# Performance work log

Measured on AMD Instinct MI355X. Metric: run time of the kernel, lower is better.

## Reference

```python
import jax, jax.numpy as jnp
import numpy as np

B = 512      # graphs per batch
NPG = 62     # nodes (electrodes) per graph
N = B * NPG  # total nodes per band
F_IN = 5     # node features
H = 8        # attention heads
C = 3        # num_classes (GATConv out channels, concat=False)
DEG = 16     # avg degree
EG = NPG * DEG
E = B * EG   # edges per band
NB = 5       # bands: delta, alpha, beta, theta, gamma
DE_DIM = 930 # 310*3


def setup_inputs() -> dict:
    key = jax.random.key(0)
    ks = jax.random.split(key, 24)
    x_bands = jax.random.normal(ks[0], (NB, N, F_IN), dtype=jnp.float32)
    # within-graph random edges: node ids in [g*62, g*62+62)
    base = (jnp.arange(B, dtype=jnp.int32) * NPG)[None, :, None]
    src = jax.random.randint(ks[1], (NB, B, EG), 0, NPG, dtype=jnp.int32) + base
    dst = jax.random.randint(ks[2], (NB, B, EG), 0, NPG, dtype=jnp.int32) + base
    edge_index_bands = jnp.stack([src.reshape(NB, E), dst.reshape(NB, E)], axis=1)  # [NB,2,E]
    batch = jnp.repeat(jnp.arange(B, dtype=jnp.int32), NPG)  # [N]
    de = jax.random.normal(ks[3], (B, NPG, 5, 3), dtype=jnp.float32)
    s = 0.3
    params = dict(
        bn_gamma=jnp.ones((NB, F_IN), jnp.float32),
        bn_beta=jnp.zeros((NB, F_IN), jnp.float32),
        W=jax.random.normal(ks[4], (NB, F_IN, H * C)) * s,
        att_src=jax.random.normal(ks[5], (NB, H, C)) * s,
        att_dst=jax.random.normal(ks[6], (NB, H, C)) * s,
        gat_bias=jax.random.normal(ks[7], (NB, C)) * 0.01,
        fg_W=jax.random.normal(ks[8], (NB * C, 64)) * s,
        fg_b=jnp.zeros((64,), jnp.float32),
        ln_g=jnp.ones((DE_DIM,), jnp.float32),
        ln_b=jnp.zeros((DE_DIM,), jnp.float32),
        q_W=jax.random.normal(ks[9], (DE_DIM, 64)) * 0.03,
        q_b=jnp.zeros((64,), jnp.float32),
        k_W=jax.random.normal(ks[10], (DE_DIM, 64)) * 0.03,
        k_b=jnp.zeros((64,), jnp.float32),
        v_W=jax.random.normal(ks[11], (DE_DIM, 64)) * 0.03,
        v_b=jnp.zeros((64,), jnp.float32),
        fa_W=jax.random.normal(ks[12], (128, C)) * s,
        fa_b=jnp.zeros((C,), jnp.float32),
    )
    return dict(x_bands=x_bands, edge_index_bands=edge_index_bands, batch=batch, de=de, **params)


def _gat_band(x, ei, g, b, Wb, a_src, a_dst, bias, batch):
    # BatchNorm1d (training-mode batch stats), eps=1e-5
    mu = x.mean(0)
    var = x.var(0)
    xn = (x - mu) * jax.lax.rsqrt(var + 1e-5) * g + b
    # GATConv(F_IN -> C, heads=H, concat=False) with self-loops
    xt = (xn @ Wb).reshape(N, H, C)                       # [N,H,C]
    al_s = (xt * a_src).sum(-1)                           # [N,H]
    al_d = (xt * a_dst).sum(-1)                           # [N,H]
    loop = jnp.arange(N, dtype=ei.dtype)
    src = jnp.concatenate([ei[0], loop])                  # [E+N]
    dst = jnp.concatenate([ei[1], loop])
    e = jax.nn.leaky_relu(al_s[src] + al_d[dst], 0.2)     # [E+N,H]
    m = jax.ops.segment_max(e, dst, num_segments=N)
    ex = jnp.exp(e - m[dst])
    denom = jax.ops.segment_sum(ex, dst, num_segments=N)  # [N,H]
    msg = ex[:, :, None] * xt[src]                        # [E+N,H,C]
    out = jax.ops.segment_sum(msg, dst, num_segments=N) / denom[:, :, None]
    out = out.mean(1) + bias                              # concat=False -> head mean
    out = jax.nn.elu(out)
    # global_mean_pool
    summed = jax.ops.segment_sum(out, batch, num_segments=B)
    cnt = jax.ops.segment_sum(jnp.ones((N,), out.dtype), batch, num_segments=B)
    return summed / cnt[:, None]                          # [B,C]


def reference(x_bands, edge_index_bands, batch, de, bn_gamma, bn_beta, W,
              att_src, att_dst, gat_bias, fg_W, fg_b, ln_g, ln_b,
              q_W, q_b, k_W, k_b, v_W, v_b, fa_W, fa_b):
    pooled = jax.vmap(_gat_band, in_axes=(0, 0, 0, 0, 0, 0, 0, 0, None))(
        x_bands, edge_index_bands, bn_gamma, bn_beta, W, att_src, att_dst, gat_bias, batch
    )  # [NB,B,C]
    x_concat = jnp.transpose(pooled, (1, 0, 2)).reshape(B, NB * C)  # [B,15]
    x_out = jax.nn.elu(x_concat @ fg_W + fg_b)                       # [B,64]
    # de branch: LayerNorm + self-attention
    de_f = de.reshape(B, DE_DIM)
    mu = de_f.mean(-1, keepdims=True)
    var = de_f.var(-1, keepdims=True)
    de_n = (de_f - mu) * jax.lax.rsqrt(var + 1e-5) * ln_g + ln_b
    Q = de_n @ q_W + q_b
    K = de_n @ k_W + k_b
    V = de_n @ v_W + v_b
    attn = jax.nn.softmax(Q @ K.T / jnp.sqrt(jnp.float32(64)), axis=-1)
    x_de = attn @ V                                                  # [B,64]
    # F.leaky_relu(x, negative_slope=1) is the identity
    out = jnp.concatenate([x_out, x_de], axis=1) @ fa_W + fa_b       # [B,3]
    return jax.nn.elu(out)
```

## Files before the change

kernel.cpp:

```cpp
#include <hip/hip_runtime.h>
#include <math.h>

#define NBANDS 5
#define BATCH  512
#define NPG    62
#define NTOT   (BATCH*NPG)
#define F_IN   5
#define NH     8
#define NC     3
#define HC     (NH*NC)
#define EG     (NPG*16)
#define ETOT   (BATCH*EG)
#define EPG    (EG+NPG)
#define DE_DIM 930
#define KS     5
#define KLEN   186
#define XTS    9
#define CSTRIDE 80
#define LOG2E  1.44269504088896340736f

#define WS_BN     0
#define WS_LNS    512
#define WS_POOLED 1536
#define WS_Q      (WS_POOLED + NBANDS*BATCH*NC)
#define WS_KT     (WS_Q  + BATCH*64)
#define WS_V      (WS_KT + BATCH*64)
#define WS_PART   (WS_V  + BATCH*64)
#define WS_END    (WS_PART + 3*KS*BATCH*64)

__device__ __forceinline__ float eluf(float x) { return x > 0.f ? x : expm1f(x); }

__global__ __launch_bounds__(256) void stats_kernel(
    const float* __restrict__ x, const float* __restrict__ de,
    float* __restrict__ ws) {
    int bid = blockIdx.x;
    int tid = threadIdx.x;
    int w = tid >> 6, lane = tid & 63;
    if (bid < 40) {
        int band = bid >> 3, chunk = bid & 7;
        const int G4 = NTOT / 8 / 4;
        const float4* xb4 =
            (const float4*)(x + (size_t)band * NTOT * F_IN) + (size_t)chunk * G4 * 5;
        float s[F_IN] = {0,0,0,0,0}, q[F_IN] = {0,0,0,0,0};
        for (int gi = tid; gi < G4; gi += 256) {
            const float4* p4 = xb4 + (size_t)gi * 5;
            float vv[20];
            *(float4*)&vv[0]  = p4[0];
            *(float4*)&vv[4]  = p4[1];
            *(float4*)&vv[8]  = p4[2];
            *(float4*)&vv[12] = p4[3];
            *(float4*)&vv[16] = p4[4];
            #pragma unroll
            for (int i = 0; i < 20; ++i) { float v = vv[i]; s[i % 5] += v; q[i % 5] += v * v; }
        }
        #pragma unroll
        for (int f = 0; f < F_IN; ++f) {
            for (int off = 32; off; off >>= 1) {
                s[f] += __shfl_down(s[f], off, 64);
                q[f] += __shfl_down(q[f], off, 64);
            }
        }
        __shared__ float part[4][10];
        if (lane == 0) {
            #pragma unroll
            for (int f = 0; f < F_IN; ++f) { part[w][f] = s[f]; part[w][5 + f] = q[f]; }
        }
        __syncthreads();
        if (tid < 10) {
            float t = part[0][tid] + part[1][tid] + part[2][tid] + part[3][tid];
            ws[WS_BN + (band * 8 + chunk) * 10 + tid] = t;
        }
    } else {
        int r = (bid - 40) * 4 + w;
        const float* row = de + (size_t)r * DE_DIM;
        float s1 = 0.f, s2 = 0.f;
        for (int i = lane; i < DE_DIM; i += 64) { float v = row[i]; s1 += v; s2 += v * v; }
        #pragma unroll
        for (int off = 32; off; off >>= 1) {
            s1 += __shfl_down(s1, off, 64);
            s2 += __shfl_down(s2, off, 64);
        }
        if (lane == 0) {
            float mu  = s1 * (1.0f / DE_DIM);
            float var = s2 * (1.0f / DE_DIM) - mu * mu;
            ws[WS_LNS + r * 2]     = mu;
            ws[WS_LNS + r * 2 + 1] = rsqrtf(var + 1e-5f);
        }
    }
}

__global__ __launch_bounds__(256) void gat_kernel(
    const float* __restrict__ x, const int* __restrict__ ei,
    const float* __restrict__ bn_g, const float* __restrict__ bn_b,
    const float* __restrict__ Wg, const float* __restrict__ attSg,
    const float* __restrict__ attDg, const float* __restrict__ biasg,
    const float* __restrict__ wsbn, float* __restrict__ pooled) {
    int g    = blockIdx.x;
    int band = blockIdx.y;
    __shared__ float4 xt4[NPG * XTS];
    __shared__ float  Wl[F_IN * HC];
    __shared__ float  attS[HC], attD[HC];
    __shared__ float  bnsum[10];
    __shared__ float  scale[F_IN], shift[F_IN];
    __shared__ float  ald[NPG * NH];
    __shared__ int    deg[NPG];
    __shared__ unsigned short csr[NPG * CSTRIDE];
    __shared__ float  outd[NPG][NC];

    int tid = threadIdx.x;
    int nbase = g * NPG;

    const int* srcp = ei + (size_t)band * 2 * ETOT + (size_t)g * EG;
    const int* dstp = srcp + ETOT;

    if (tid < F_IN * HC) Wl[tid] = Wg[band * F_IN * HC + tid];
    if (tid >= 128 && tid < 128 + HC) attS[tid - 128] = attSg[band * HC + tid - 128];
    if (tid >= 160 && tid < 160 + HC) attD[tid - 160] = attDg[band * HC + tid - 160];
    if (tid < NPG) deg[tid] = 0;
    if (tid >= 192 && tid < 202) {
        int f = tid - 192;
        float t = 0.f;
        #pragma unroll
        for (int c = 0; c < 8; ++c) t += wsbn[(band * 8 + c) * 10 + f];
        bnsum[f] = t;
    }
    if (tid >= 192 && tid < 192 + F_IN) {
        int f = tid - 192;
        float mu  = bnsum[f] * (1.0f / NTOT);
        float var = bnsum[5 + f] * (1.0f / NTOT) - mu * mu;
        float sc  = rsqrtf(var + 1e-5f) * bn_g[band * F_IN + f];
        scale[f] = sc;
        shift[f] = bn_b[band * F_IN + f] - mu * sc;
    }
    __syncthreads();

    for (int e = tid; e < EG; e += 256) {
        int ls = srcp[e] - nbase;
        int ld = dstp[e] - nbase;
        int k = atomicAdd(&deg[ld], 1);
        if (k < CSTRIDE - 1) csr[ld * CSTRIDE + 1 + k] = (unsigned short)(ls * XTS);
    }
    if (tid < NPG) csr[tid * CSTRIDE] = (unsigned short)(tid * XTS);
    for (int p = tid; p < NPG * NH; p += 256) {
        int n = p >> 3, h = p & 7;
        const float* xr = x + (size_t)band * NTOT * F_IN + (size_t)(nbase + n) * F_IN;
        float c0 = 0.f, c1 = 0.f, c2 = 0.f;
        #pragma unroll
        for (int f = 0; f < F_IN; ++f) {
            float xv = xr[f] * scale[f] + shift[f];
            c0 += xv * Wl[f * HC + h * NC + 0];
            c1 += xv * Wl[f * HC + h * NC + 1];
            c2 += xv * Wl[f * HC + h * NC + 2];
        }
        float as = c0 * attS[h * NC] + c1 * attS[h * NC + 1] + c2 * attS[h * NC + 2];
        float ad = c0 * attD[h * NC] + c1 * attD[h * NC + 1] + c2 * attD[h * NC + 2];
        xt4[n * XTS + h] = make_float4(c0, c1, c2, as * LOG2E);
        ald[p] = ad * LOG2E;
    }
    __syncthreads();

    for (int p = tid; p < NPG * NH; p += 256) {
        int d = p >> 3, h = p & 7;
        int s0 = d * CSTRIDE;
        int s1 = s0 + 1 + deg[d];
        float adv = ald[p];
        float den = 0.f, m0 = 0.f, m1 = 0.f, m2 = 0.f;
        #pragma unroll 2
        for (int e = s0; e < s1; ++e) {
            float4 t = xt4[csr[e] + h];
            float v = t.w + adv;
            v = fmaxf(v, 0.2f * v);
            float ex = exp2f(v);
            den += ex;
            m0 += ex * t.x;
            m1 += ex * t.y;
            m2 += ex * t.z;
        }
        float rd = 1.0f / den;
        float o0 = m0 * rd, o1 = m1 * rd, o2 = m2 * rd;
        #pragma unroll
        for (int off = 1; off < 8; off <<= 1) {
            o0 += __shfl_xor(o0, off, 64);
            o1 += __shfl_xor(o1, off, 64);
            o2 += __shfl_xor(o2, off, 64);
        }
        if (h == 0) { outd[d][0] = o0; outd[d][1] = o1; outd[d][2] = o2; }
    }
    __syncthreads();

    float oc[NC] = {0.f, 0.f, 0.f};
    if (tid < NPG) {
        #pragma unroll
        for (int c = 0; c < NC; ++c)
            oc[c] = eluf(outd[tid][c] * (1.0f / NH) + biasg[band * NC + c]);
    }
    if (tid < 64) {
        #pragma unroll
        for (int c = 0; c < NC; ++c) {
            float v = oc[c];
            for (int off = 32; off; off >>= 1) v += __shfl_down(v, off, 64);
            if (tid == 0)
                pooled[((size_t)band * BATCH + g) * NC + c] = v * (1.0f / NPG);
        }
    }
}

__global__ __launch_bounds__(256) void qkv_partial(
    const float* __restrict__ de, const float* __restrict__ lns,
    const float* __restrict__ ln_g, const float* __restrict__ ln_b,
    const float* __restrict__ qW, const float* __restrict__ kW,
    const float* __restrict__ vW, float* __restrict__ part) {
    int rt = blockIdx.x;
    int m  = blockIdx.y;
    int ks = blockIdx.z;
    __shared__ float dl[4][KLEN];
    int tid = threadIdx.x, w = tid >> 6, col = tid & 63;
    for (int i = tid; i < 4 * KLEN; i += 256) {
        int rr = i / KLEN, ii = i - rr * KLEN;
        int row = rt * 4 + rr, gcol = ks * KLEN + ii;
        float mu = lns[row * 2], rstd = lns[row * 2 + 1];
        dl[rr][ii] = (de[(size_t)row * DE_DIM + gcol] - mu) * rstd * ln_g[gcol] + ln_b[gcol];
    }
    __syncthreads();
    const float* Wm = ((m == 0) ? qW : (m == 1) ? kW : vW) + (size_t)ks * KLEN * 64;
    float a[6] = {0, 0, 0, 0, 0, 0};
    for (int i = 0; i < KLEN; i += 6) {
        #pragma unroll
        for (int j = 0; j < 6; ++j)
            a[j] += dl[w][i + j] * Wm[(size_t)(i + j) * 64 + col];
    }
    float acc = ((a[0] + a[1]) + (a[2] + a[3])) + (a[4] + a[5]);
    part[(((size_t)m * KS + ks) * BATCH + rt * 4 + w) * 64 + col] = acc;
}

__global__ __launch_bounds__(256) void qkv_reduce(
    const float* __restrict__ part,
    const float* __restrict__ qb, const float* __restrict__ kb,
    const float* __restrict__ vb,
    float* __restrict__ Q, float* __restrict__ KT, float* __restrict__ V) {
    int idx = blockIdx.x * 256 + threadIdx.x;
    int m  = idx >> 15;
    int local = idx & 32767;
    if (m == 1) {
        int row = local & 511, col = local >> 9;
        float s = 0.f;
        #pragma unroll
        for (int ks = 0; ks < KS; ++ks)
            s += part[(((size_t)KS + ks) << 15) + (row << 6) + col];
        KT[local] = s + kb[col];
    } else {
        int col = local & 63;
        float s = 0.f;
        #pragma unroll
        for (int ks = 0; ks < KS; ++ks)
            s += part[(((size_t)m * KS + ks) << 15) + local];
        s += (m == 0) ? qb[col] : vb[col];
        ((m == 0) ? Q : V)[local] = s;
    }
}

__global__ __launch_bounds__(256) void qkv_fused_fb(
    const float* __restrict__ de, const float* __restrict__ ln_g,
    const float* __restrict__ ln_b,
    const float* __restrict__ qW, const float* __restrict__ qb,
    const float* __restrict__ kW, const float* __restrict__ kb,
    const float* __restrict__ vW, const float* __restrict__ vb,
    float* __restrict__ Q, float* __restrict__ KT, float* __restrict__ V) {
    int r0 = blockIdx.x * 4;
    int m  = blockIdx.y;
    __shared__ float dn[4][DE_DIM];
    int tid  = threadIdx.x;
    int w    = tid >> 6, lane = tid & 63;
    const float* row = de + (size_t)(r0 + w) * DE_DIM;
    float s1 = 0.f, s2 = 0.f;
    for (int i = lane; i < DE_DIM; i += 64) {
        float v = row[i]; dn[w][i] = v; s1 += v; s2 += v * v;
    }
    #pragma unroll
    for (int off = 32; off; off >>= 1) {
        s1 += __shfl_down(s1, off, 64);
        s2 += __shfl_down(s2, off, 64);
    }
    float mu   = __shfl(s1, 0, 64) * (1.0f / DE_DIM);
    float var  = __shfl(s2, 0, 64) * (1.0f / DE_DIM) - mu * mu;
    float rstd = rsqrtf(var + 1e-5f);
    for (int i = lane; i < DE_DIM; i += 64)
        dn[w][i] = (dn[w][i] - mu) * rstd * ln_g[i] + ln_b[i];
    __syncthreads();
    const float* Wm = (m == 0) ? qW : (m == 1) ? kW : vW;
    const float* bm = (m == 0) ? qb : (m == 1) ? kb : vb;
    float a[10];
    #pragma unroll
    for (int j = 0; j < 10; ++j) a[j] = 0.f;
    for (int i = 0; i < DE_DIM; i += 10) {
        #pragma unroll
        for (int j = 0; j < 10; ++j)
            a[j] += dn[w][i + j] * Wm[(size_t)(i + j) * 64 + lane];
    }
    float acc = (((a[0] + a[1]) + (a[2] + a[3])) + ((a[4] + a[5]) + (a[6] + a[7])))
              + (a[8] + a[9]) + bm[lane];
    int r = r0 + w;
    if (m == 1) KT[lane * BATCH + r] = acc;
    else ((m == 0) ? Q : V)[(size_t)r * 64 + lane] = acc;
}

__global__ __launch_bounds__(256) void attn_final(
    const float* __restrict__ Q, const float* __restrict__ KT,
    const float* __restrict__ V, const float* __restrict__ pooled,
    const float* __restrict__ fgW, const float* __restrict__ fgb,
    const float* __restrict__ faW, const float* __restrict__ fab,
    float* __restrict__ out) {
    int b = blockIdx.x;
    int tid = threadIdx.x;
    __shared__ float qrow[64];
    __shared__ float p[BATCH];
    __shared__ float red[8];
    __shared__ float pv[4][64];
    __shared__ float xde[64], xout[64];
    if (tid < 64) qrow[tid] = Q[(size_t)b * 64 + tid];
    __syncthreads();

    float a0 = 0.f, a1 = 0.f, b0 = 0.f, b1 = 0.f;
    #pragma unroll 8
    for (int i = 0; i < 64; i += 2) {
        float q0 = qrow[i], q1 = qrow[i + 1];
        a0 += q0 * KT[(size_t)i * BATCH + tid];
        a1 += q1 * KT[(size_t)(i + 1) * BATCH + tid];
        b0 += q0 * KT[(size_t)i * BATCH + tid + 256];
        b1 += q1 * KT[(size_t)(i + 1) * BATCH + tid + 256];
    }
    float sj0 = (a0 + a1) * 0.125f, sj1 = (b0 + b1) * 0.125f;

    float mx = fmaxf(sj0, sj1);
    for (int off = 32; off; off >>= 1) mx = fmaxf(mx, __shfl_down(mx, off, 64));
    if ((tid & 63) == 0) red[tid >> 6] = mx;
    __syncthreads();
    mx = fmaxf(fmaxf(red[0], red[1]), fmaxf(red[2], red[3]));
    float e0 = __expf(sj0 - mx), e1 = __expf(sj1 - mx);
    p[tid] = e0; p[tid + 256] = e1;
    float s = e0 + e1;
    for (int off = 32; off; off >>= 1) s += __shfl_down(s, off, 64);
    if ((tid & 63) == 0) red[4 + (tid >> 6)] = s;
    __syncthreads();
    float denom = red[4] + red[5] + red[6] + red[7];

    int o = tid & 63, cq = tid >> 6;
    float acc = 0.f;
    #pragma unroll 4
    for (int j = cq * 128; j < cq * 128 + 128; ++j)
        acc += p[j] * V[(size_t)j * 64 + o];
    pv[cq][o] = acc;
    __syncthreads();
    if (tid < 64)
        xde[tid] = (pv[0][tid] + pv[1][tid] + pv[2][tid] + pv[3][tid]) / denom;
    if (tid >= 64 && tid < 128) {
        int oo = tid - 64;
        float a = fgb[oo];
        #pragma unroll
        for (int j = 0; j < NBANDS * NC; ++j) {
            int band = j / NC, c = j % NC;
            a += pooled[((size_t)band * BATCH + b) * NC + c] * fgW[j * 64 + oo];
        }
        xout[oo] = eluf(a);
    }
    __syncthreads();
    if (tid < NC) {
        float a = fab[tid];
        for (int i = 0; i < 64; ++i) a += xout[i] * faW[i * NC + tid];
        for (int i = 0; i < 64; ++i) a += xde[i] * faW[(64 + i) * NC + tid];
        out[(size_t)b * NC + tid] = eluf(a);
    }
}

extern "C" void kernel_launch(void* const* d_in, const int* in_sizes, int n_in,
                              void* d_out, int out_size, void* d_ws, size_t ws_size,
                              hipStream_t stream) {
    const float* x     = (const float*)d_in[0];
    const int*   ei    = (const int*)  d_in[1];
    const float* de    = (const float*)d_in[3];
    const float* bn_g  = (const float*)d_in[4];
    const float* bn_b  = (const float*)d_in[5];
    const float* W     = (const float*)d_in[6];
    const float* attS  = (const float*)d_in[7];
    const float* attD  = (const float*)d_in[8];
    const float* gbias = (const float*)d_in[9];
    const float* fgW   = (const float*)d_in[10];
    const float* fgb   = (const float*)d_in[11];
    const float* ln_g  = (const float*)d_in[12];
    const float* ln_b  = (const float*)d_in[13];
    const float* qW    = (const float*)d_in[14];
    const float* qb    = (const float*)d_in[15];
    const float* kW    = (const float*)d_in[16];
    const float* kb    = (const float*)d_in[17];
    const float* vW    = (const float*)d_in[18];
    const float* vb    = (const float*)d_in[19];
    const float* faW   = (const float*)d_in[20];
    const float* fab   = (const float*)d_in[21];
    float* ws  = (float*)d_ws;
    float* out = (float*)d_out;

    stats_kernel<<<168, 256, 0, stream>>>(x, de, ws);
    gat_kernel<<<dim3(BATCH, NBANDS), 256, 0, stream>>>(
        x, ei, bn_g, bn_b, W, attS, attD, gbias, ws + WS_BN, ws + WS_POOLED);

    if (ws_size >= (size_t)WS_END * sizeof(float)) {
        qkv_partial<<<dim3(BATCH / 4, 3, KS), 256, 0, stream>>>(
            de, ws + WS_LNS, ln_g, ln_b, qW, kW, vW, ws + WS_PART);
        qkv_reduce<<<(3 * BATCH * 64) / 256, 256, 0, stream>>>(
            ws + WS_PART, qb, kb, vb, ws + WS_Q, ws + WS_KT, ws + WS_V);
    } else {
        qkv_fused_fb<<<dim3(BATCH / 4, 3), 256, 0, stream>>>(
            de, ln_g, ln_b, qW, qb, kW, kb, vW, vb,
            ws + WS_Q, ws + WS_KT, ws + WS_V);
    }
    attn_final<<<BATCH, 256, 0, stream>>>(ws + WS_Q, ws + WS_KT, ws + WS_V,
                                          ws + WS_POOLED, fgW, fgb, faW, fab, out);
}
```

Before: 67.63 us.

## Replace QKV split-K reduce kernel with atomic accumulation into bias-initialized buffers

Removes the qkv_reduce launch. stats_kernel gains extra blocks that pre-fill the Q, K and V buffers with their biases, and qkv_partial then atomically adds its split-K partial sums straight into them. K is now stored row-major instead of transposed, so attn_final computes scores with float4 loads along each K row. This saves a kernel launch and the partial-buffer round trip, at the cost of float atomics with non-deterministic summation order and strided per-thread K reads in attn_final.

```diff
diff --git a/kernel.cpp b/kernel.cpp
--- a/kernel.cpp
+++ b/kernel.cpp
@@ -23,16 +23,16 @@
 #define WS_LNS    512
 #define WS_POOLED 1536
 #define WS_Q      (WS_POOLED + NBANDS*BATCH*NC)
-#define WS_KT     (WS_Q  + BATCH*64)
-#define WS_V      (WS_KT + BATCH*64)
-#define WS_PART   (WS_V  + BATCH*64)
-#define WS_END    (WS_PART + 3*KS*BATCH*64)
+#define WS_K      (WS_Q + BATCH*64)
+#define WS_V      (WS_K + BATCH*64)
+#define WS_END    (WS_V + BATCH*64)
 
 __device__ __forceinline__ float eluf(float x) { return x > 0.f ? x : expm1f(x); }
 
 __global__ __launch_bounds__(256) void stats_kernel(
     const float* __restrict__ x, const float* __restrict__ de,
-    float* __restrict__ ws) {
+    const float* __restrict__ qb, const float* __restrict__ kb,
+    const float* __restrict__ vb, float* __restrict__ ws) {
     int bid = blockIdx.x;
     int tid = threadIdx.x;
     int w = tid >> 6, lane = tid & 63;
@@ -70,7 +70,7 @@
             float t = part[0][tid] + part[1][tid] + part[2][tid] + part[3][tid];
             ws[WS_BN + (band * 8 + chunk) * 10 + tid] = t;
         }
-    } else {
+    } else if (bid < 168) {
         int r = (bid - 40) * 4 + w;
         const float* row = de + (size_t)r * DE_DIM;
         float s1 = 0.f, s2 = 0.f;
@@ -86,6 +86,11 @@
             ws[WS_LNS + r * 2]     = mu;
             ws[WS_LNS + r * 2 + 1] = rsqrtf(var + 1e-5f);
         }
+    } else {
+        int idx = (bid - 168) * 256 + tid;
+        int m = idx >> 15, local = idx & 32767, col = local & 63;
+        const float* bm = (m == 0) ? qb : (m == 1) ? kb : vb;
+        ws[((m == 0) ? WS_Q : (m == 1) ? WS_K : WS_V) + local] = bm[col];
     }
 }
 
@@ -209,7 +214,8 @@
     const float* __restrict__ de, const float* __restrict__ lns,
     const float* __restrict__ ln_g, const float* __restrict__ ln_b,
     const float* __restrict__ qW, const float* __restrict__ kW,
-    const float* __restrict__ vW, float* __restrict__ part) {
+    const float* __restrict__ vW,
+    float* __restrict__ Q, float* __restrict__ K, float* __restrict__ V) {
     int rt = blockIdx.x;
     int m  = blockIdx.y;
     int ks = blockIdx.z;
@@ -230,33 +236,8 @@
             a[j] += dl[w][i + j] * Wm[(size_t)(i + j) * 64 + col];
     }
     float acc = ((a[0] + a[1]) + (a[2] + a[3])) + (a[4] + a[5]);
-    part[(((size_t)m * KS + ks) * BATCH + rt * 4 + w) * 64 + col] = acc;
-}
-
-__global__ __launch_bounds__(256) void qkv_reduce(
-    const float* __restrict__ part,
-    const float* __restrict__ qb, const float* __restrict__ kb,
-    const float* __restrict__ vb,
-    float* __restrict__ Q, float* __restrict__ KT, float* __restrict__ V) {
-    int idx = blockIdx.x * 256 + threadIdx.x;
-    int m  = idx >> 15;
-    int local = idx & 32767;
-    if (m == 1) {
-        int row = local & 511, col = local >> 9;
-        float s = 0.f;
-        #pragma unroll
-        for (int ks = 0; ks < KS; ++ks)
-            s += part[(((size_t)KS + ks) << 15) + (row << 6) + col];
-        KT[local] = s + kb[col];
-    } else {
-        int col = local & 63;
-        float s = 0.f;
-        #pragma unroll
-        for (int ks = 0; ks < KS; ++ks)
-            s += part[(((size_t)m * KS + ks) << 15) + local];
-        s += (m == 0) ? qb[col] : vb[col];
-        ((m == 0) ? Q : V)[local] = s;
-    }
+    float* Om = (m == 0) ? Q : (m == 1) ? K : V;
+    atomicAdd(&Om[(size_t)(rt * 4 + w) * 64 + col], acc);
 }
 
 __global__ __launch_bounds__(256) void qkv_fused_fb(
@@ -265,7 +246,7 @@
     const float* __restrict__ qW, const float* __restrict__ qb,
     const float* __restrict__ kW, const float* __restrict__ kb,
     const float* __restrict__ vW, const float* __restrict__ vb,
-    float* __restrict__ Q, float* __restrict__ KT, float* __restrict__ V) {
+    float* __restrict__ Q, float* __restrict__ K, float* __restrict__ V) {
     int r0 = blockIdx.x * 4;
     int m  = blockIdx.y;
     __shared__ float dn[4][DE_DIM];
@@ -299,13 +280,12 @@
     }
     float acc = (((a[0] + a[1]) + (a[2] + a[3])) + ((a[4] + a[5]) + (a[6] + a[7])))
               + (a[8] + a[9]) + bm[lane];
-    int r = r0 + w;
-    if (m == 1) KT[lane * BATCH + r] = acc;
-    else ((m == 0) ? Q : V)[(size_t)r * 64 + lane] = acc;
+    float* Om = (m == 0) ? Q : (m == 1) ? K : V;
+    Om[(size_t)(r0 + w) * 64 + lane] = acc;
 }
 
 __global__ __launch_bounds__(256) void attn_final(
-    const float* __restrict__ Q, const float* __restrict__ KT,
+    const float* __restrict__ Q, const float* __restrict__ K,
     const float* __restrict__ V, const float* __restrict__ pooled,
     const float* __restrict__ fgW, const float* __restrict__ fgb,
     const float* __restrict__ faW, const float* __restrict__ fab,
@@ -320,23 +300,26 @@
     if (tid < 64) qrow[tid] = Q[(size_t)b * 64 + tid];
     __syncthreads();
 
-    float a0 = 0.f, a1 = 0.f, b0 = 0.f, b1 = 0.f;
-    #pragma unroll 8
-    for (int i = 0; i < 64; i += 2) {
-        float q0 = qrow[i], q1 = qrow[i + 1];
-        a0 += q0 * KT[(size_t)i * BATCH + tid];
-        a1 += q1 * KT[(size_t)(i + 1) * BATCH + tid];
-        b0 += q0 * KT[(size_t)i * BATCH + tid + 256];
-        b1 += q1 * KT[(size_t)(i + 1) * BATCH + tid + 256];
-    }
-    float sj0 = (a0 + a1) * 0.125f, sj1 = (b0 + b1) * 0.125f;
-
-    float mx = fmaxf(sj0, sj1);
+    float sj[2];
+    #pragma unroll
+    for (int r = 0; r < 2; ++r) {
+        int j = tid + r * 256;
+        const float4* k4 = (const float4*)(K + (size_t)j * 64);
+        float a = 0.f;
+        #pragma unroll
+        for (int i = 0; i < 16; ++i) {
+            float4 kv = k4[i];
+            a += qrow[4*i]   * kv.x + qrow[4*i+1] * kv.y
+               + qrow[4*i+2] * kv.z + qrow[4*i+3] * kv.w;
+        }
+        sj[r] = a * 0.125f;
+    }
+    float mx = fmaxf(sj[0], sj[1]);
     for (int off = 32; off; off >>= 1) mx = fmaxf(mx, __shfl_down(mx, off, 64));
     if ((tid & 63) == 0) red[tid >> 6] = mx;
     __syncthreads();
     mx = fmaxf(fmaxf(red[0], red[1]), fmaxf(red[2], red[3]));
-    float e0 = __expf(sj0 - mx), e1 = __expf(sj1 - mx);
+    float e0 = __expf(sj[0] - mx), e1 = __expf(sj[1] - mx);
     p[tid] = e0; p[tid + 256] = e1;
     float s = e0 + e1;
     for (int off = 32; off; off >>= 1) s += __shfl_down(s, off, 64);
@@ -399,20 +382,19 @@
     float* ws  = (float*)d_ws;
     float* out = (float*)d_out;
 
-    stats_kernel<<<168, 256, 0, stream>>>(x, de, ws);
+    stats_kernel<<<168 + 384, 256, 0, stream>>>(x, de, qb, kb, vb, ws);
     gat_kernel<<<dim3(BATCH, NBANDS), 256, 0, stream>>>(
         x, ei, bn_g, bn_b, W, attS, attD, gbias, ws + WS_BN, ws + WS_POOLED);
 
     if (ws_size >= (size_t)WS_END * sizeof(float)) {
         qkv_partial<<<dim3(BATCH / 4, 3, KS), 256, 0, stream>>>(
-            de, ws + WS_LNS, ln_g, ln_b, qW, kW, vW, ws + WS_PART);
-        qkv_reduce<<<(3 * BATCH * 64) / 256, 256, 0, stream>>>(
-            ws + WS_PART, qb, kb, vb, ws + WS_Q, ws + WS_KT, ws + WS_V);
+            de, ws + WS_LNS, ln_g, ln_b, qW, kW, vW,
+            ws + WS_Q, ws + WS_K, ws + WS_V);
     } else {
         qkv_fused_fb<<<dim3(BATCH / 4, 3), 256, 0, stream>>>(
             de, ln_g, ln_b, qW, qb, kW, kb, vW, vb,
-            ws + WS_Q, ws + WS_KT, ws + WS_V);
-    }
-    attn_final<<<BATCH, 256, 0, stream>>>(ws + WS_Q, ws + WS_KT, ws + WS_V,
+            ws + WS_Q, ws + WS_K, ws + WS_V);
+    }
+    attn_final<<<BATCH, 256, 0, stream>>>(ws + WS_Q, ws + WS_K, ws + WS_V,
                                           ws + WS_POOLED, fgW, fgb, faW, fab, out);
 }
```

After: 68.91 us. Within noise of the previous version (+1.9%).
